# Kernel tuning notes

Hardware: AMD Instinct MI355X
Metric: run time of the kernel (lower is better)

## Reference

```python
import jax, jax.numpy as jnp
import numpy as np

# cfg constants (init_kwargs)
NMS_THRESH = 0.6
CONF_THRESH = 0.05
TOPN = 1000           # nms_thresh_topN: pre-NMS cap and post-NMS cap
NUM_CLASSES = 80
CLS_OFFSET = 4096.0   # > max image coord; class-aware NMS via coordinate offset


def setup_inputs() -> dict:
    key = jax.random.key(0)
    k0, k1, k2, k3 = jax.random.split(key, 4)
    B, H, W, C = 16, 128, 128, NUM_CLASSES
    N = H * W
    image_h, image_w = 1024, 1024
    # anchor-point pixel coordinates for this FPN level
    locations = jax.random.uniform(k0, (N, 2), dtype=jnp.float32) * 1024.0
    pred_cls = jax.random.normal(k1, (B, H, W, C), dtype=jnp.float32)
    # (l, t, r, b) distances are positive
    pred_boxes = jax.random.uniform(k2, (B, H, W, 4), dtype=jnp.float32) * 64.0
    pred_centerness = jax.random.normal(k3, (B, H, W), dtype=jnp.float32)
    return {"locations": locations, "pred_cls": pred_cls, "pred_boxes": pred_boxes,
            "pred_centerness": pred_centerness, "image_h": image_h, "image_w": image_w}


def _pairwise_iou(b):  # b: [K, 4] xyxy
    x1, y1, x2, y2 = b[:, 0], b[:, 1], b[:, 2], b[:, 3]
    area = jnp.maximum(x2 - x1, 0.0) * jnp.maximum(y2 - y1, 0.0)
    ix1 = jnp.maximum(x1[:, None], x1[None, :])
    iy1 = jnp.maximum(y1[:, None], y1[None, :])
    ix2 = jnp.minimum(x2[:, None], x2[None, :])
    iy2 = jnp.minimum(y2[:, None], y2[None, :])
    inter = jnp.maximum(ix2 - ix1, 0.0) * jnp.maximum(iy2 - iy1, 0.0)
    return inter / (area[:, None] + area[None, :] - inter + 1e-9)


def _nms_keep(iou, valid):
    # greedy NMS over score-descending candidates; iou: [B,K,K], valid: [B,K] bool
    K = iou.shape[-1]
    ar = jnp.arange(K)

    def body(i, keep):
        iou_i = jax.lax.dynamic_index_in_dim(iou, i, axis=1, keepdims=False)  # [B,K]
        keep_i = jnp.take(keep, i, axis=1)                                    # [B]
        sup = (iou_i > NMS_THRESH) & (ar[None, :] > i) & keep_i[:, None]
        return keep & ~sup

    return jax.lax.fori_loop(0, K, body, valid)


def reference(locations, pred_cls, pred_boxes, pred_centerness, image_h, image_w):
    B, H, W, C = pred_cls.shape
    N = H * W
    cls = jax.nn.sigmoid(pred_cls.reshape(B, N, C))
    ctr = jax.nn.sigmoid(pred_centerness.reshape(B, N))
    boxes = pred_boxes.reshape(B, N, 4)
    scores = cls * ctr[:, :, None]                    # [B,N,C]
    mask = cls > CONF_THRESH
    neg = jnp.asarray(-jnp.inf, scores.dtype)
    flat = jnp.where(mask, scores, neg).reshape(B, N * C)
    # pre-NMS top-K over masked (location, class) candidates; emulates
    # cls_mask_top_n = clamp(mask.sum(), max=topN) + topk in the torch code
    vals, idx = jax.lax.top_k(flat, TOPN)             # [B,K]
    valid = jnp.isfinite(vals)
    loc_i = idx // C                                  # location index
    lab = idx % C + 1                                 # 1-based class label
    pb = jnp.take_along_axis(boxes, loc_i[:, :, None], axis=1)   # [B,K,4] (l,t,r,b)
    locs = locations[loc_i]                                       # [B,K,2]
    x1 = jnp.clip(locs[..., 0] - pb[..., 0], 0.0, image_w - 1)
    y1 = jnp.clip(locs[..., 1] - pb[..., 1], 0.0, image_h - 1)
    x2 = jnp.clip(locs[..., 0] + pb[..., 2], 0.0, image_w - 1)
    y2 = jnp.clip(locs[..., 1] + pb[..., 3], 0.0, image_h - 1)
    det = jnp.stack([x1, y1, x2, y2], axis=-1)        # [B,K,4] xyxy, clipped
    score = jnp.where(valid, vals, 0.0)
    # sort by score descending for greedy NMS
    order = jnp.argsort(-score, axis=1)
    score = jnp.take_along_axis(score, order, axis=1)
    valid = jnp.take_along_axis(valid, order, axis=1)
    lab = jnp.take_along_axis(lab, order, axis=1)
    det = jnp.take_along_axis(det, order[:, :, None], axis=1)
    # per-class NMS via class-offset trick (boxes of different classes never overlap)
    iou = jax.vmap(_pairwise_iou)(det + lab.astype(det.dtype)[:, :, None] * CLS_OFFSET)
    keep = _nms_keep(iou, valid) & valid
    # final topN (nms_thresh_topN) is a no-op here: candidates <= TOPN already
    boxes_out = det * keep[:, :, None].astype(det.dtype)
    scores_out = jnp.where(keep, score, 0.0)
    labels_out = jnp.where(keep, lab, 0)
    return boxes_out, scores_out, labels_out
```

## Files before the change

### kernel.cpp

```cpp
#include <hip/hip_runtime.h>

#define B_    16
#define N_    16384
#define C_    80
#define NC_   (N_ * C_)
#define TOPN_ 1000
#define T0_   0.70f
#define T0KEY_ 0x3F333333u
#define RKEY_  0x3E800000u
#define NBIN_  4096
#define BLKCAP_ 128
#define RESCCAP_ 8192

#define OFF_CNT    0u
#define OFF_CAND   16384u
#define OFF_RESC   (16384u + 4194304u)

__device__ __forceinline__ float sigm(float x) { return 1.0f / (1.0f + expf(-x)); }

__device__ __forceinline__ int binof(unsigned key) {
    int b = (int)((key - RKEY_) >> 12);
    return b > (NBIN_ - 1) ? (NBIN_ - 1) : b;
}
__device__ __forceinline__ unsigned key_lb(int b) {
    return RKEY_ + ((unsigned)b << 12);
}

__global__ __launch_bounds__(256, 4) void k_pass1(const float* __restrict__ cls,
                                                  const float* __restrict__ ctr,
                                                  unsigned* __restrict__ cnt,
                                                  unsigned long long* __restrict__ cand) {
    __shared__ float xh[64];
    __shared__ float sbv[64];
    __shared__ unsigned long long stage[BLKCAP_];
    __shared__ unsigned lcnt;
    const int blk = blockIdx.x, t = threadIdx.x;
    const int b = blk >> 8, k = blk & 255;
    if (t == 0) lcnt = 0;
    if (t < 64) {
        float sc = sigm(ctr[b * N_ + k * 64 + t]);
        sbv[t] = sc;
        float q = T0_ / sc;
        xh[t] = (q < 1.f) ? (logf(q / (1.f - q)) - 1e-3f) : 3.0e38f;
    }
    __syncthreads();
    const float4* p = (const float4*)(cls + (size_t)b * NC_ + (size_t)k * 5120);
    float4 v[5];
    #pragma unroll
    for (int i = 0; i < 5; ++i) v[i] = p[5 * t + i];
    const int r = t >> 2;
    const float thr = xh[r];
    float mx = v[0].x;
    #pragma unroll
    for (int i = 0; i < 5; ++i)
        mx = fmaxf(mx, fmaxf(fmaxf(v[i].x, v[i].y), fmaxf(v[i].z, v[i].w)));
    if (mx >= thr) {
        const float sb = sbv[r];
        #pragma unroll
        for (int i = 0; i < 5; ++i) {
            float xs[4] = {v[i].x, v[i].y, v[i].z, v[i].w};
            #pragma unroll
            for (int j = 0; j < 4; ++j) {
                if (xs[j] >= thr) {
                    float sapx = sb * __builtin_amdgcn_rcpf(1.f + __expf(-xs[j]));
                    if (sapx >= T0_ * 0.999f) {
                        float s = sigm(xs[j]);
                        unsigned key = __float_as_uint(s * sb);
                        if (key >= T0KEY_) {
                            unsigned pos = atomicAdd(&lcnt, 1u);
                            if (pos < (unsigned)BLKCAP_) {
                                unsigned e = (unsigned)(k * 5120 + (5 * t + i) * 4 + j);
                                stage[pos] = ((unsigned long long)key << 32) |
                                             (unsigned long long)(0xFFFFFFFFu - e);
                            }
                        }
                    }
                }
            }
        }
    }
    __syncthreads();
    unsigned lc = lcnt; if (lc > (unsigned)BLKCAP_) lc = (unsigned)BLKCAP_;
    if (t == 0) cnt[blk] = lc;
    unsigned long long* seg = cand + ((size_t)blk << 7);
    for (unsigned i = t; i < lc; i += 256) seg[i] = stage[i];
}

union TailSMem {
    struct {
        unsigned hbin[NBIN_];
        unsigned binBase[NBIN_];
        unsigned long long srt[2048];
        unsigned long long srt2[1024];
    } s;
    struct {
        float4 bxo[1024];
        unsigned short clsList[1024];
        unsigned clsStart[81];
        unsigned clsCur[81];
        unsigned short supIdx[1024 * 16];
        unsigned char nsup[1024];
    } c;
};

__global__ __launch_bounds__(1024) void k_tail(
        const unsigned long long* __restrict__ cand, const unsigned* __restrict__ cnt,
        unsigned long long* __restrict__ resc,
        const float* __restrict__ boxes, const float* __restrict__ locs,
        const int* __restrict__ ph, const int* __restrict__ pw,
        const float* __restrict__ cls, const float* __restrict__ ctr,
        float* __restrict__ out) {
    __shared__ TailSMem u;
    __shared__ unsigned csh[256];
    __shared__ unsigned Lsh, totSh, rcnt, rcwSh;
    __shared__ unsigned long long keepw[16];
    __shared__ unsigned long long vmaskSh[16];
    const int b = blockIdx.x, t = threadIdx.x;

    if (t == 0) { rcnt = 0; rcwSh = 0; }
    if (t < 256) {
        unsigned cc = cnt[b * 256 + t];
        csh[t] = cc > (unsigned)BLKCAP_ ? (unsigned)BLKCAP_ : cc;
    }
    __syncthreads();
    if (t < 64) {
        unsigned s4 = csh[4 * t] + csh[4 * t + 1] + csh[4 * t + 2] + csh[4 * t + 3];
        #pragma unroll
        for (int off = 32; off >= 1; off >>= 1) s4 += __shfl_down(s4, off, 64);
        if (t == 0) totSh = s4;
    }
    __syncthreads();
    if (totSh < (unsigned)TOPN_) {
        unsigned long long* rsw = resc + ((size_t)b << 13);
        const float4* p = (const float4*)(cls + (size_t)b * NC_);
        for (unsigned f = t; f < (unsigned)(NC_ / 4); f += 1024) {
            float4 v = p[f];
            unsigned nl = f / 20;
            float sb = sigm(ctr[b * N_ + nl]);
            float xs[4] = {v.x, v.y, v.z, v.w};
            #pragma unroll
            for (int j = 0; j < 4; ++j) {
                float s = sigm(xs[j]);
                if (s > 0.05f) {
                    unsigned key = __float_as_uint(s * sb);
                    if (key >= RKEY_ && key < T0KEY_) {
                        unsigned pos = atomicAdd(&rcnt, 1u);
                        if (pos < (unsigned)RESCCAP_) {
                            unsigned e = 4u * f + (unsigned)j;
                            rsw[pos] = ((unsigned long long)key << 32) |
                                       (unsigned long long)(0xFFFFFFFFu - e);
                        }
                    }
                }
            }
        }
        __syncthreads();
        if (t == 0) {
            unsigned rc = rcnt;
            rcwSh = rc > (unsigned)RESCCAP_ ? (unsigned)RESCCAP_ : rc;
        }
        __syncthreads();
    }

    #pragma unroll
    for (int i = 0; i < 4; ++i) u.s.hbin[t + 1024 * i] = 0;
    u.s.srt[t] = 0ull; u.s.srt[t + 1024] = 0ull;
    u.s.srt2[t] = 0ull;
    __syncthreads();
    const unsigned long long* g = cand + ((size_t)b << 15);
    const unsigned long long* rs = resc + ((size_t)b << 13);
    const unsigned rcw = rcwSh;
    {
        const int s = t >> 2;
        const unsigned cc = csh[s];
        const unsigned long long* gs = g + ((size_t)s << 7);
        for (unsigned o = 2u * (unsigned)(t & 3); o < cc; o += 8) {
            unsigned long long c0 = gs[o];
            unsigned long long c1 = (o + 1 < cc) ? gs[o + 1] : 0ull;
            atomicAdd(&u.s.hbin[binof((unsigned)(c0 >> 32))], 1u);
            if (o + 1 < cc)
                atomicAdd(&u.s.hbin[binof((unsigned)(c1 >> 32))], 1u);
        }
    }
    for (unsigned o = t; o < rcw; o += 1024)
        atomicAdd(&u.s.hbin[binof((unsigned)(rs[o] >> 32))], 1u);
    __syncthreads();
    if (t < 64) {
        const int l = t;
        unsigned cs = 0;
        for (int i = 0; i < 64; ++i) cs += u.s.hbin[64 * l + i];
        unsigned S = cs;
        #pragma unroll
        for (int off = 1; off < 64; off <<= 1) {
            unsigned y = __shfl_down(S, off, 64);
            if (l + off < 64) S += y;
        }
        unsigned acc = S - cs;
        int bc_l = NBIN_;
        for (int b2 = 63; b2 >= 0; --b2) {
            int bin = 64 * l + b2;
            u.s.binBase[bin] = acc;
            if (acc < (unsigned)TOPN_) bc_l = bin;
            acc += u.s.hbin[bin];
        }
        #pragma unroll
        for (int off = 1; off < 64; off <<= 1) {
            int y = __shfl_down(bc_l, off, 64);
            bc_l = bc_l < y ? bc_l : y;
        }
        if (l == 0) Lsh = key_lb(bc_l < NBIN_ ? bc_l : 0);
    }
    __syncthreads();
    const unsigned Lk = Lsh;
    {
        const int s = t >> 2;
        const unsigned cc = csh[s];
        const unsigned long long* gs = g + ((size_t)s << 7);
        for (unsigned o = 2u * (unsigned)(t & 3); o < cc; o += 8) {
            unsigned long long c0 = gs[o];
            unsigned long long c1 = (o + 1 < cc) ? gs[o + 1] : 0ull;
            unsigned k0 = (unsigned)(c0 >> 32);
            if (k0 >= Lk) {
                unsigned slot = atomicAdd(&u.s.binBase[binof(k0)], 1u);
                if (slot < 2048u) u.s.srt[slot] = c0;
            }
            if (o + 1 < cc) {
                unsigned k1 = (unsigned)(c1 >> 32);
                if (k1 >= Lk) {
                    unsigned slot = atomicAdd(&u.s.binBase[binof(k1)], 1u);
                    if (slot < 2048u) u.s.srt[slot] = c1;
                }
            }
        }
    }
    for (unsigned o = t; o < rcw; o += 1024) {
        unsigned long long comp = rs[o];
        unsigned key = (unsigned)(comp >> 32);
        if (key >= Lk) {
            unsigned slot = atomicAdd(&u.s.binBase[binof(key)], 1u);
            if (slot < 2048u) u.s.srt[slot] = comp;
        }
    }
    __syncthreads();
    #pragma unroll
    for (int pp = 0; pp < 2; ++pp) {
        unsigned p = (unsigned)t + 1024u * pp;
        unsigned long long comp = u.s.srt[p];
        if (comp) {
            int bin = binof((unsigned)(comp >> 32));
            unsigned endq = u.s.binBase[bin];
            unsigned pop = u.s.hbin[bin];
            unsigned beg = endq - pop;
            unsigned end2 = endq > 2048u ? 2048u : endq;
            unsigned rank = 0;
            for (unsigned j = beg; j < end2; ++j) rank += (u.s.srt[j] > comp);
            unsigned pos = beg + rank;
            if (pos < 1024u) u.s.srt2[pos] = comp;
        }
    }
    __syncthreads();
    unsigned long long comp = u.s.srt2[t];
    unsigned key = (unsigned)(comp >> 32);
    float4 d = {0.f, 0.f, 0.f, 0.f}, doff = {0.f, 0.f, 0.f, 0.f};
    float sc = 0.f; int lb = 0;
    if (key) {
        unsigned idx = 0xFFFFFFFFu - (unsigned)comp;
        unsigned loc = idx / (unsigned)C_;
        unsigned cc2 = idx - loc * (unsigned)C_;
        lb = (int)cc2 + 1;
        float4 pb = ((const float4*)boxes)[(size_t)b * N_ + loc];
        float lx = locs[2 * loc], ly = locs[2 * loc + 1];
        float Wm1 = (float)(pw[0] - 1), Hm1 = (float)(ph[0] - 1);
        d.x = fminf(fmaxf(lx - pb.x, 0.f), Wm1);
        d.y = fminf(fmaxf(ly - pb.y, 0.f), Hm1);
        d.z = fminf(fmaxf(lx + pb.z, 0.f), Wm1);
        d.w = fminf(fmaxf(ly + pb.w, 0.f), Hm1);
        sc = __uint_as_float(key);
        float off = (float)lb * 4096.0f;
        doff.x = d.x + off; doff.y = d.y + off; doff.z = d.z + off; doff.w = d.w + off;
    }
    const bool valid = (key != 0u);
    {
        unsigned long long ball = __ballot(valid);
        if ((t & 63) == 0) vmaskSh[t >> 6] = ball;
    }
    __syncthreads();

    u.c.bxo[t] = doff;
    if (t < 81) u.c.clsStart[t] = 0;
    __syncthreads();
    if (lb > 0) atomicAdd(&u.c.clsStart[lb], 1u);
    __syncthreads();
    if (t < 64) {
        const int l = t;
        unsigned s0 = 0, s1 = 0;
        if (l < 40) { s0 = u.c.clsStart[2 * l + 1]; s1 = u.c.clsStart[2 * l + 2]; }
        unsigned p = s0 + s1;
        unsigned S = p;
        #pragma unroll
        for (int off = 1; off < 64; off <<= 1) {
            unsigned y = __shfl_up(S, off, 64);
            if (l >= off) S += y;
        }
        unsigned excl = S - p;
        if (l < 40) {
            u.c.clsStart[2 * l + 1] = excl;
            u.c.clsCur[2 * l + 1]   = excl;
            u.c.clsStart[2 * l + 2] = excl + s0;
            u.c.clsCur[2 * l + 2]   = excl + s0;
        }
    }
    __syncthreads();
    if (lb > 0) {
        unsigned pos = atomicAdd(&u.c.clsCur[lb], 1u);
        u.c.clsList[pos] = (unsigned short)t;
    }
    __syncthreads();
    unsigned nsup = 0;
    if (valid) {
        float4 A = doff;
        float aA = fmaxf(A.z - A.x, 0.f) * fmaxf(A.w - A.y, 0.f);
        unsigned beg = u.c.clsStart[lb], end = u.c.clsCur[lb];
        for (unsigned q = beg; q < end; ++q) {
            int j = (int)u.c.clsList[q];
            if (j < t) {
                float4 Bv = u.c.bxo[j];
                float aB = fmaxf(Bv.z - Bv.x, 0.f) * fmaxf(Bv.w - Bv.y, 0.f);
                float ix1 = fmaxf(A.x, Bv.x), iy1 = fmaxf(A.y, Bv.y);
                float ix2 = fminf(A.z, Bv.z), iy2 = fminf(A.w, Bv.w);
                float inter = fmaxf(ix2 - ix1, 0.f) * fmaxf(iy2 - iy1, 0.f);
                float iou = inter / (aA + aB - inter + 1e-9f);
                if (iou > 0.6f) {
                    if (nsup < 16u) u.c.supIdx[t * 16 + nsup] = (unsigned short)j;
                    ++nsup;
                }
            }
        }
        if (nsup > 16u) nsup = 16u;
    }
    u.c.nsup[t] = (unsigned char)nsup;
    __syncthreads();

    if (t < 64) {
        const int ii = t;
        for (int gg = 0; gg < 16; ++gg) {
            const int row = gg * 64 + ii;
            const unsigned base = (unsigned)(gg << 6);
            unsigned ns = u.c.nsup[row];
            unsigned long long diag = 0;
            bool supP = false;
            for (unsigned q = 0; q < ns; ++q) {
                unsigned j = (unsigned)u.c.supIdx[row * 16 + q];
                if (j < base) {
                    if ((keepw[j >> 6] >> (j & 63)) & 1ull) supP = true;
                } else {
                    diag |= 1ull << (j & 63);
                }
            }
            bool alive = (((vmaskSh[gg] >> ii) & 1ull) != 0) && !supP;
            unsigned long long undec = __ballot(alive);
            unsigned long long kept = 0;
            while (undec) {
                bool meU = ((undec >> ii) & 1ull) != 0;
                bool supK = (kept & diag) != 0;
                bool anyU = (undec & diag) != 0;
                unsigned long long bkm = __ballot(meU && !supK && !anyU);
                unsigned long long brm = __ballot(meU && supK);
                kept |= bkm;
                undec &= ~(bkm | brm);
            }
            if (ii == 0) keepw[gg] = kept;
        }
    }
    __syncthreads();

    if (t < TOPN_) {
        bool kp = ((keepw[t >> 6] >> (t & 63)) & 1ull) != 0;
        ((float4*)out)[(size_t)b * TOPN_ + t] = kp ? d : make_float4(0.f, 0.f, 0.f, 0.f);
        out[B_ * TOPN_ * 4 + b * TOPN_ + t] = kp ? sc : 0.f;
        out[B_ * TOPN_ * 5 + b * TOPN_ + t] = kp ? (float)lb : 0.f;
    }
}

extern "C" void kernel_launch(void* const* d_in, const int* in_sizes, int n_in,
                              void* d_out, int out_size, void* d_ws, size_t ws_size,
                              hipStream_t stream) {
    (void)in_sizes; (void)n_in; (void)out_size; (void)ws_size;
    const float* locations = (const float*)d_in[0];
    const float* pred_cls  = (const float*)d_in[1];
    const float* pred_box  = (const float*)d_in[2];
    const float* pred_ctr  = (const float*)d_in[3];
    const int*   ph        = (const int*)d_in[4];
    const int*   pw        = (const int*)d_in[5];
    float* out = (float*)d_out;

    char* w = (char*)d_ws;
    unsigned* cnt            = (unsigned*)(w + OFF_CNT);
    unsigned long long* cand = (unsigned long long*)(w + OFF_CAND);
    unsigned long long* resc = (unsigned long long*)(w + OFF_RESC);


    k_pass1<<<4096, 256, 0, stream>>>(pred_cls, pred_ctr, cnt, cand);
    k_tail<<<B_, 1024, 0, stream>>>(cand, cnt, resc, pred_box, locations, ph, pw,
                                    pred_cls, pred_ctr, out);
}
```

Measured before the change: 167.9 us.

## Fuse candidate pass and tail into one kernel via last-block-done counter

Merges the threshold-filter pass and the per-image sort/NMS tail into a single kernel. 1024 blocks of 1024 threads each filter a 256-row slice, write candidates, then bump a per-image atomic counter, and the last block for each image runs the tail. This removes one kernel launch and the gap between the two kernels. In exchange it adds a memset launch, uses larger blocks with heavy shared memory for the filter phase (which lowers occupancy), and serialises the tail behind the last-arriving block.

```diff
diff --git a/kernel.cpp b/kernel.cpp
--- a/kernel.cpp
+++ b/kernel.cpp
@@ -9,12 +9,15 @@
 #define T0KEY_ 0x3F333333u
 #define RKEY_  0x3E800000u
 #define NBIN_  4096
-#define BLKCAP_ 128
+#define NBLKB_ 64
+#define BLKCAP_ 512
 #define RESCCAP_ 8192
 
-#define OFF_CNT    0u
-#define OFF_CAND   16384u
-#define OFF_RESC   (16384u + 4194304u)
+#define OFF_DONE   0u
+#define ZERO_BYTES 1024u
+#define OFF_CNT    1024u
+#define OFF_CAND   5120u
+#define OFF_RESC   (5120u + 4194304u)
 
 __device__ __forceinline__ float sigm(float x) { return 1.0f / (1.0f + expf(-x)); }
 
@@ -26,67 +29,12 @@
     return RKEY_ + ((unsigned)b << 12);
 }
 
-__global__ __launch_bounds__(256, 4) void k_pass1(const float* __restrict__ cls,
-                                                  const float* __restrict__ ctr,
-                                                  unsigned* __restrict__ cnt,
-                                                  unsigned long long* __restrict__ cand) {
-    __shared__ float xh[64];
-    __shared__ float sbv[64];
-    __shared__ unsigned long long stage[BLKCAP_];
-    __shared__ unsigned lcnt;
-    const int blk = blockIdx.x, t = threadIdx.x;
-    const int b = blk >> 8, k = blk & 255;
-    if (t == 0) lcnt = 0;
-    if (t < 64) {
-        float sc = sigm(ctr[b * N_ + k * 64 + t]);
-        sbv[t] = sc;
-        float q = T0_ / sc;
-        xh[t] = (q < 1.f) ? (logf(q / (1.f - q)) - 1e-3f) : 3.0e38f;
-    }
-    __syncthreads();
-    const float4* p = (const float4*)(cls + (size_t)b * NC_ + (size_t)k * 5120);
-    float4 v[5];
-    #pragma unroll
-    for (int i = 0; i < 5; ++i) v[i] = p[5 * t + i];
-    const int r = t >> 2;
-    const float thr = xh[r];
-    float mx = v[0].x;
-    #pragma unroll
-    for (int i = 0; i < 5; ++i)
-        mx = fmaxf(mx, fmaxf(fmaxf(v[i].x, v[i].y), fmaxf(v[i].z, v[i].w)));
-    if (mx >= thr) {
-        const float sb = sbv[r];
-        #pragma unroll
-        for (int i = 0; i < 5; ++i) {
-            float xs[4] = {v[i].x, v[i].y, v[i].z, v[i].w};
-            #pragma unroll
-            for (int j = 0; j < 4; ++j) {
-                if (xs[j] >= thr) {
-                    float sapx = sb * __builtin_amdgcn_rcpf(1.f + __expf(-xs[j]));
-                    if (sapx >= T0_ * 0.999f) {
-                        float s = sigm(xs[j]);
-                        unsigned key = __float_as_uint(s * sb);
-                        if (key >= T0KEY_) {
-                            unsigned pos = atomicAdd(&lcnt, 1u);
-                            if (pos < (unsigned)BLKCAP_) {
-                                unsigned e = (unsigned)(k * 5120 + (5 * t + i) * 4 + j);
-                                stage[pos] = ((unsigned long long)key << 32) |
-                                             (unsigned long long)(0xFFFFFFFFu - e);
-                            }
-                        }
-                    }
-                }
-            }
-        }
-    }
-    __syncthreads();
-    unsigned lc = lcnt; if (lc > (unsigned)BLKCAP_) lc = (unsigned)BLKCAP_;
-    if (t == 0) cnt[blk] = lc;
-    unsigned long long* seg = cand + ((size_t)blk << 7);
-    for (unsigned i = t; i < lc; i += 256) seg[i] = stage[i];
-}
-
 union TailSMem {
+    struct {
+        float xh[256];
+        float sbv[256];
+        unsigned long long stage[BLKCAP_];
+    } p;
     struct {
         unsigned hbin[NBIN_];
         unsigned binBase[NBIN_];
@@ -103,28 +51,92 @@
     } c;
 };
 
-__global__ __launch_bounds__(1024) void k_tail(
-        const unsigned long long* __restrict__ cand, const unsigned* __restrict__ cnt,
-        unsigned long long* __restrict__ resc,
+__global__ __launch_bounds__(1024) void k_fused(
+        const float* __restrict__ cls, const float* __restrict__ ctr,
         const float* __restrict__ boxes, const float* __restrict__ locs,
         const int* __restrict__ ph, const int* __restrict__ pw,
-        const float* __restrict__ cls, const float* __restrict__ ctr,
+        unsigned* __restrict__ done, unsigned* __restrict__ cnt,
+        unsigned long long* __restrict__ cand, unsigned long long* __restrict__ resc,
         float* __restrict__ out) {
     __shared__ TailSMem u;
-    __shared__ unsigned csh[256];
-    __shared__ unsigned Lsh, totSh, rcnt, rcwSh;
+    __shared__ unsigned csh[NBLKB_];
+    __shared__ unsigned lcnt, lastSh, Lsh, totSh, rcnt, rcwSh;
     __shared__ unsigned long long keepw[16];
     __shared__ unsigned long long vmaskSh[16];
-    const int b = blockIdx.x, t = threadIdx.x;
+    const int blk = blockIdx.x, t = threadIdx.x;
+    const int b = blk >> 6, k2 = blk & 63;
+
+    if (t == 0) lcnt = 0;
+    if (t < 256) {
+        int row = k2 * 256 + t;
+        float sc = sigm(ctr[b * N_ + row]);
+        u.p.sbv[t] = sc;
+        float q = T0_ / sc;
+        u.p.xh[t] = (q < 1.f) ? (logf(q / (1.f - q)) - 1e-3f) : 3.0e38f;
+    }
+    __syncthreads();
+    {
+        const float4* pc = (const float4*)(cls + (size_t)b * NC_ + (size_t)k2 * 20480);
+        float4 v[5];
+        #pragma unroll
+        for (int i = 0; i < 5; ++i) v[i] = pc[5 * t + i];
+        const int r = t >> 2;
+        const float thr = u.p.xh[r];
+        float mx = v[0].x;
+        #pragma unroll
+        for (int i = 0; i < 5; ++i)
+            mx = fmaxf(mx, fmaxf(fmaxf(v[i].x, v[i].y), fmaxf(v[i].z, v[i].w)));
+        if (mx >= thr) {
+            const float sb = u.p.sbv[r];
+            #pragma unroll
+            for (int i = 0; i < 5; ++i) {
+                float xs[4] = {v[i].x, v[i].y, v[i].z, v[i].w};
+                #pragma unroll
+                for (int j = 0; j < 4; ++j) {
+                    if (xs[j] >= thr) {
+                        float sapx = sb * __builtin_amdgcn_rcpf(1.f + __expf(-xs[j]));
+                        if (sapx >= T0_ * 0.999f) {
+                            float s = sigm(xs[j]);
+                            unsigned key = __float_as_uint(s * sb);
+                            if (key >= T0KEY_) {
+                                unsigned pos = atomicAdd(&lcnt, 1u);
+                                if (pos < (unsigned)BLKCAP_) {
+                                    unsigned e = (unsigned)(k2 * 20480 + (5 * t + i) * 4 + j);
+                                    u.p.stage[pos] = ((unsigned long long)key << 32) |
+                                                     (unsigned long long)(0xFFFFFFFFu - e);
+                                }
+                            }
+                        }
+                    }
+                }
+            }
+        }
+    }
+    __syncthreads();
+    {
+        unsigned lc = lcnt; if (lc > (unsigned)BLKCAP_) lc = (unsigned)BLKCAP_;
+        if (t == 0) cnt[blk] = lc;
+        unsigned long long* seg = cand + ((size_t)blk << 9);
+        for (unsigned i = t; i < lc; i += 1024) seg[i] = u.p.stage[i];
+    }
+    __threadfence();
+    __syncthreads();
+    if (t == 0) {
+        unsigned old = atomicAdd(&done[b * 16], 1u);
+        lastSh = (old == (unsigned)(NBLKB_ - 1)) ? 1u : 0u;
+    }
+    __syncthreads();
+    if (!lastSh) return;
+    __threadfence();
 
     if (t == 0) { rcnt = 0; rcwSh = 0; }
-    if (t < 256) {
-        unsigned cc = cnt[b * 256 + t];
+    if (t < NBLKB_) {
+        unsigned cc = cnt[b * NBLKB_ + t];
         csh[t] = cc > (unsigned)BLKCAP_ ? (unsigned)BLKCAP_ : cc;
     }
     __syncthreads();
     if (t < 64) {
-        unsigned s4 = csh[4 * t] + csh[4 * t + 1] + csh[4 * t + 2] + csh[4 * t + 3];
+        unsigned s4 = csh[t];
         #pragma unroll
         for (int off = 32; off >= 1; off >>= 1) s4 += __shfl_down(s4, off, 64);
         if (t == 0) totSh = s4;
@@ -132,9 +144,9 @@
     __syncthreads();
     if (totSh < (unsigned)TOPN_) {
         unsigned long long* rsw = resc + ((size_t)b << 13);
-        const float4* p = (const float4*)(cls + (size_t)b * NC_);
+        const float4* pc = (const float4*)(cls + (size_t)b * NC_);
         for (unsigned f = t; f < (unsigned)(NC_ / 4); f += 1024) {
-            float4 v = p[f];
+            float4 v = pc[f];
             unsigned nl = f / 20;
             float sb = sigm(ctr[b * N_ + nl]);
             float xs[4] = {v.x, v.y, v.z, v.w};
@@ -171,10 +183,10 @@
     const unsigned long long* rs = resc + ((size_t)b << 13);
     const unsigned rcw = rcwSh;
     {
-        const int s = t >> 2;
+        const int s = t >> 4;
         const unsigned cc = csh[s];
-        const unsigned long long* gs = g + ((size_t)s << 7);
-        for (unsigned o = 2u * (unsigned)(t & 3); o < cc; o += 8) {
+        const unsigned long long* gs = g + ((size_t)s << 9);
+        for (unsigned o = 2u * (unsigned)(t & 15); o < cc; o += 32) {
             unsigned long long c0 = gs[o];
             unsigned long long c1 = (o + 1 < cc) ? gs[o + 1] : 0ull;
             atomicAdd(&u.s.hbin[binof((unsigned)(c0 >> 32))], 1u);
@@ -213,10 +225,10 @@
     __syncthreads();
     const unsigned Lk = Lsh;
     {
-        const int s = t >> 2;
+        const int s = t >> 4;
         const unsigned cc = csh[s];
-        const unsigned long long* gs = g + ((size_t)s << 7);
-        for (unsigned o = 2u * (unsigned)(t & 3); o < cc; o += 8) {
+        const unsigned long long* gs = g + ((size_t)s << 9);
+        for (unsigned o = 2u * (unsigned)(t & 15); o < cc; o += 32) {
             unsigned long long c0 = gs[o];
             unsigned long long c1 = (o + 1 < cc) ? gs[o + 1] : 0ull;
             unsigned k0 = (unsigned)(c0 >> 32);
@@ -395,12 +407,14 @@
     float* out = (float*)d_out;
 
     char* w = (char*)d_ws;
+    unsigned* done           = (unsigned*)(w + OFF_DONE);
     unsigned* cnt            = (unsigned*)(w + OFF_CNT);
     unsigned long long* cand = (unsigned long long*)(w + OFF_CAND);
     unsigned long long* resc = (unsigned long long*)(w + OFF_RESC);
 
-
-    k_pass1<<<4096, 256, 0, stream>>>(pred_cls, pred_ctr, cnt, cand);
-    k_tail<<<B_, 1024, 0, stream>>>(cand, cnt, resc, pred_box, locations, ph, pw,
-                                    pred_cls, pred_ctr, out);
+    hipMemsetAsync(w, 0, ZERO_BYTES, stream);
+
+    k_fused<<<B_ * NBLKB_, 1024, 0, stream>>>(pred_cls, pred_ctr, pred_box,
+                                              locations, ph, pw, done, cnt,
+                                              cand, resc, out);
 }
```

Result: slower. 541.0 us (+222.3%).
